# Kernel tuning notes

Hardware: AMD Instinct MI355X
Metric: run time of the kernel (lower is better)

## Reference

```python
import jax, jax.numpy as jnp
import numpy as np

B, S, DX, DH = 8, 4096, 1024, 1024

def setup_inputs() -> dict:
    key = jax.random.key(0)
    ks = jax.random.split(key, 7)
    s_x = 1.0 / np.sqrt(DX)
    s_h = 1.0 / np.sqrt(DH)
    return {
        "x":  jax.random.normal(ks[0], (B, S, DX), dtype=jnp.float32),
        "Wz": jax.random.uniform(ks[1], (DH, DX), jnp.float32, -s_x, s_x),
        "bz": jax.random.uniform(ks[2], (DH,),   jnp.float32, -s_x, s_x),
        "Wh": jax.random.uniform(ks[3], (DH, DX), jnp.float32, -s_x, s_x),
        "bh": jax.random.uniform(ks[4], (DH,),   jnp.float32, -s_x, s_x),
        "Wo": jax.random.uniform(ks[5], (DX, DH), jnp.float32, -s_h, s_h),
        "bo": jax.random.uniform(ks[6], (DX,),   jnp.float32, -s_h, s_h),
    }

def log_g(x):
    # Appendix B.3 of "Were RNNs All We Needed?"
    return jnp.where(x >= 0, jnp.log(jax.nn.relu(x) + 0.5), -jax.nn.softplus(-x))

def parallel_scan_log(log_coeffs, log_values):
    # Heinsen log-space associative scan: h_t = a_t * h_{t-1} + b_t (h_0 = 0)
    a_star = jnp.cumsum(log_coeffs, axis=1)                       # [B,S,H]
    log_h = a_star + jax.lax.cumlogsumexp(log_values - a_star, axis=1)
    return jnp.exp(log_h)

def reference(x, Wz, bz, Wh, bh, Wo, bo):
    k       = jnp.einsum('bsd,hd->bsh', x, Wz) + bz               # pre-gate
    tilde_h = jnp.einsum('bsd,hd->bsh', x, Wh) + bh               # candidate
    log_z           = -jax.nn.softplus(-k)                        # log sigmoid(k)
    log_one_minus_z = -jax.nn.softplus(k)                         # log sigmoid(-k)
    log_tilde_h     = log_g(tilde_h)
    h = parallel_scan_log(log_one_minus_z, log_z + log_tilde_h)   # [B,S,H]
    out = jnp.einsum('bsh,dh->bsd', h, Wo) + bo                   # [B,S,DX]
    return out
```

## Files before the change

### kernel.cpp

```cpp
#include <hip/hip_runtime.h>
#include <stdint.h>
#include <stddef.h>


typedef __bf16 bf16;
typedef __bf16 bf16x8 __attribute__((ext_vector_type(8)));
typedef float f32x4 __attribute__((ext_vector_type(4)));

#define DEV __device__ __forceinline__

DEV void gload_lds16(const bf16* g, bf16* l) {
  __builtin_amdgcn_global_load_lds((const __attribute__((address_space(1))) void*)g,
                                   (__attribute__((address_space(3))) void*)l,
                                   16, 0, 0);
}

__global__ __launch_bounds__(256)
void conv_b(const float* __restrict__ src, bf16* __restrict__ dst, int n4) {
  const int stride = gridDim.x * 256;
  for (int i = blockIdx.x * 256 + threadIdx.x; i < n4; i += stride) {
    float4 v = ((const float4*)src)[i];
    bf16 o[4] = {(bf16)v.x, (bf16)v.y, (bf16)v.z, (bf16)v.w};
    *(uint64_t*)(dst + 4 * (size_t)i) = *(uint64_t*)o;
  }
}

__global__ __launch_bounds__(256, 2)
void gate_gemm(const bf16* __restrict__ X,
               const bf16* __restrict__ Wz, const bf16* __restrict__ Wh,
               const float* __restrict__ bzf, const float* __restrict__ bhf,
               bf16* __restrict__ aB, bf16* __restrict__ vB) {
  __shared__ __align__(16) bf16 As [128 * 32];
  __shared__ __align__(16) bf16 Bzs[128 * 32];
  __shared__ __align__(16) bf16 Bhs[128 * 32];

  const int lane = threadIdx.x & 63;
  const int wave = threadIdx.x >> 6;
  const int wm = wave >> 1, wn = wave & 1;
  const int tileM = blockIdx.y * 128;
  const int tileN = blockIdx.x * 128;
  const int q = lane >> 4, r = lane & 15;
  const int srow = lane >> 2;
  const int scol = (lane & 3) * 8;

  const bf16* ga[2]; const bf16* gz[2]; const bf16* gh[2];
  bf16* la[2]; bf16* lz[2]; bf16* lh[2];
#pragma unroll
  for (int j = 0; j < 2; ++j) {
    const int cid = j * 4 + wave;
    const int row = cid * 16 + srow;
    ga[j] = X  + (size_t)(tileM + row) * 1024 + scol;
    gz[j] = Wz + (size_t)(tileN + row) * 1024 + scol;
    gh[j] = Wh + (size_t)(tileN + row) * 1024 + scol;
    la[j] = As  + cid * 512;
    lz[j] = Bzs + cid * 512;
    lh[j] = Bhs + cid * 512;
  }

  const bf16* pA[4]; const bf16* pBz[4]; const bf16* pBh[4];
#pragma unroll
  for (int f = 0; f < 4; ++f) {
    pA[f]  = As  + (wm * 64 + f * 16 + r) * 32 + q * 8;
    pBz[f] = Bzs + (wn * 64 + f * 16 + r) * 32 + q * 8;
    pBh[f] = Bhs + (wn * 64 + f * 16 + r) * 32 + q * 8;
  }

  f32x4 accz[4][4], acch[4][4];
#pragma unroll
  for (int i = 0; i < 4; ++i)
#pragma unroll
    for (int j = 0; j < 4; ++j) {
      accz[i][j] = (f32x4){0.f, 0.f, 0.f, 0.f};
      acch[i][j] = (f32x4){0.f, 0.f, 0.f, 0.f};
    }

  for (int k0 = 0; k0 < 1024; k0 += 32) {
    __syncthreads();
#pragma unroll
    for (int j = 0; j < 2; ++j) {
      gload_lds16(ga[j] + k0, la[j]);
      gload_lds16(gz[j] + k0, lz[j]);
      gload_lds16(gh[j] + k0, lh[j]);
    }
    __syncthreads();

    bf16x8 af[4];
#pragma unroll
    for (int fm = 0; fm < 4; ++fm) af[fm] = *(const bf16x8*)pA[fm];
#pragma unroll
    for (int fn = 0; fn < 4; ++fn) {
      bf16x8 bz8 = *(const bf16x8*)pBz[fn];
      bf16x8 bh8 = *(const bf16x8*)pBh[fn];
#pragma unroll
      for (int fm = 0; fm < 4; ++fm) {
        accz[fm][fn] = __builtin_amdgcn_mfma_f32_16x16x32_bf16(af[fm], bz8, accz[fm][fn], 0, 0, 0);
        acch[fm][fn] = __builtin_amdgcn_mfma_f32_16x16x32_bf16(af[fm], bh8, acch[fm][fn], 0, 0, 0);
      }
    }
  }

#pragma unroll
  for (int fn = 0; fn < 4; ++fn) {
    const int n = tileN + wn * 64 + fn * 16 + r;
    const float bzv = bzf[n], bhv = bhf[n];
#pragma unroll
    for (int fm = 0; fm < 4; ++fm) {
      const int m0 = tileM + wm * 64 + fm * 16 + q * 4;
#pragma unroll
      for (int i = 0; i < 4; ++i) {
        float kv = accz[fm][fn][i] + bzv;
        float tv = acch[fm][fn][i] + bhv;
        float e   = __expf(-kv);
        float inv = 1.f / (1.f + e);
        float a   = e * inv;
        float g   = (tv >= 0.f) ? (tv + 0.5f) : (1.f / (1.f + __expf(-tv)));
        size_t idx = (size_t)(m0 + i) * 1024 + n;
        aB[idx] = (bf16)a;
        vB[idx] = (bf16)(inv * g);
      }
    }
  }
}

__global__ __launch_bounds__(256)
void chk_gate(const bf16* __restrict__ X,
              const bf16* __restrict__ Wz, const bf16* __restrict__ Wh,
              const float* __restrict__ bzf, const float* __restrict__ bhf,
              const bf16* __restrict__ aB, const bf16* __restrict__ vB,
              int* __restrict__ badA) {
  int i = blockIdx.x * 256 + threadIdx.x;
  int m = (i * 12347) & 32767;
  int n = (i * 4099) & 1023;
  float kz = 0.f, kh = 0.f;
  for (int k = 0; k < 1024; ++k) {
    float xv = (float)X[(size_t)m * 1024 + k];
    kz = fmaf(xv, (float)Wz[(size_t)n * 1024 + k], kz);
    kh = fmaf(xv, (float)Wh[(size_t)n * 1024 + k], kh);
  }
  kz += bzf[n]; kh += bhf[n];
  float e = __expf(-kz), inv = 1.f / (1.f + e);
  float a = e * inv;
  float g = (kh >= 0.f) ? (kh + 0.5f) : (1.f / (1.f + __expf(-kh)));
  float v = inv * g;
  size_t idx = (size_t)m * 1024 + n;
  int ok = (fabsf((float)aB[idx] - a) <= 0.04f) &&
           (fabsf((float)vB[idx] - v) <= 0.08f);
  if (!ok) atomicAdd(badA, 1);
}

__global__ __launch_bounds__(256)
void fb_gate(const int* __restrict__ badA, const bf16* __restrict__ X,
             const bf16* __restrict__ Wz, const bf16* __restrict__ Wh,
             const float* __restrict__ bzf, const float* __restrict__ bhf,
             bf16* __restrict__ aB, bf16* __restrict__ vB) {
  if (*badA < 4) return;
  const int n = (blockIdx.x & 3) * 256 + threadIdx.x;
  const int m0 = (blockIdx.x >> 2) * 16;
  for (int mi = 0; mi < 16; ++mi) {
    const int m = m0 + mi;
    float kz = 0.f, kh = 0.f;
    for (int k = 0; k < 1024; ++k) {
      float xv = (float)X[(size_t)m * 1024 + k];
      kz = fmaf(xv, (float)Wz[(size_t)n * 1024 + k], kz);
      kh = fmaf(xv, (float)Wh[(size_t)n * 1024 + k], kh);
    }
    kz += bzf[n]; kh += bhf[n];
    float e = __expf(-kz), inv = 1.f / (1.f + e);
    float a = e * inv;
    float g = (kh >= 0.f) ? (kh + 0.5f) : (1.f / (1.f + __expf(-kh)));
    size_t idx = (size_t)m * 1024 + n;
    aB[idx] = (bf16)a;
    vB[idx] = (bf16)(inv * g);
  }
}

__global__ __launch_bounds__(256)
void scan_phase1(const bf16* __restrict__ aB, const bf16* __restrict__ vB,
                 float* __restrict__ Ac, float* __restrict__ Vc) {
  const int tid = blockIdx.x * 256 + threadIdx.x;
  const int hg = tid & 127, c = (tid >> 7) & 63, b = tid >> 13;
  const size_t base = (size_t)(b * 4096 + c * 64) * 1024 + hg * 8;
  float A[8], V[8];
#pragma unroll
  for (int j = 0; j < 8; ++j) { A[j] = 1.f; V[j] = 0.f; }
#pragma unroll 8
  for (int t = 0; t < 64; ++t) {
    bf16x8 a8 = *(const bf16x8*)(aB + base + (size_t)t * 1024);
    bf16x8 v8 = *(const bf16x8*)(vB + base + (size_t)t * 1024);
#pragma unroll
    for (int j = 0; j < 8; ++j) {
      float a = (float)a8[j];
      V[j] = fmaf(a, V[j], (float)v8[j]);
      A[j] *= a;
    }
  }
  const size_t o = (size_t)(b * 64 + c) * 1024 + hg * 8;
#pragma unroll
  for (int j = 0; j < 8; ++j) { Ac[o + j] = A[j]; Vc[o + j] = V[j]; }
}

__global__ __launch_bounds__(256)
void scan_phase2(const float* __restrict__ Ac, const float* __restrict__ Vc,
                 float* __restrict__ Hin) {
  const int tid = blockIdx.x * 256 + threadIdx.x;
  const int h = tid & 1023, b = tid >> 10;
  float carry = 0.f;
  for (int c = 0; c < 64; ++c) {
    const int idx = (b * 64 + c) * 1024 + h;
    Hin[idx] = carry;
    carry = fmaf(Ac[idx], carry, Vc[idx]);
  }
}

__global__ __launch_bounds__(256)
void scan_phase3(const bf16* __restrict__ aB, const bf16* vB,
                 const float* __restrict__ Hin, bf16* hB) {
  const int tid = blockIdx.x * 256 + threadIdx.x;
  const int hg = tid & 127, c = (tid >> 7) & 63, b = tid >> 13;
  const size_t base = (size_t)(b * 4096 + c * 64) * 1024 + hg * 8;
  const size_t o = (size_t)(b * 64 + c) * 1024 + hg * 8;
  float hc[8];
#pragma unroll
  for (int j = 0; j < 8; ++j) hc[j] = Hin[o + j];
#pragma unroll 4
  for (int t = 0; t < 64; ++t) {
    bf16x8 a8 = *(const bf16x8*)(aB + base + (size_t)t * 1024);
    bf16x8 v8 = *(const bf16x8*)(vB + base + (size_t)t * 1024);
    bf16x8 h8;
#pragma unroll
    for (int j = 0; j < 8; ++j) {
      hc[j] = fmaf((float)a8[j], hc[j], (float)v8[j]);
      h8[j] = (bf16)hc[j];
    }
    *(bf16x8*)(hB + base + (size_t)t * 1024) = h8;
  }
}

__global__ __launch_bounds__(256, 2)
void out_gemm(const bf16* __restrict__ H, const bf16* __restrict__ Wo,
              const float* __restrict__ bof, float* __restrict__ O) {
  __shared__ __align__(16) bf16 As[128 * 32];
  __shared__ __align__(16) bf16 Bs[128 * 32];

  const int lane = threadIdx.x & 63;
  const int wave = threadIdx.x >> 6;
  const int wm = wave >> 1, wn = wave & 1;
  const int tileM = blockIdx.y * 128;
  const int tileN = blockIdx.x * 128;
  const int q = lane >> 4, r = lane & 15;
  const int srow = lane >> 2;
  const int scol = (lane & 3) * 8;

  const bf16* ga[2]; const bf16* gb[2]; bf16* la[2]; bf16* lb[2];
#pragma unroll
  for (int j = 0; j < 2; ++j) {
    const int cid = j * 4 + wave;
    const int row = cid * 16 + srow;
    ga[j] = H  + (size_t)(tileM + row) * 1024 + scol;
    gb[j] = Wo + (size_t)(tileN + row) * 1024 + scol;
    la[j] = As + cid * 512;
    lb[j] = Bs + cid * 512;
  }
  const bf16* pA[4]; const bf16* pB[4];
#pragma unroll
  for (int f = 0; f < 4; ++f) {
    pA[f] = As + (wm * 64 + f * 16 + r) * 32 + q * 8;
    pB[f] = Bs + (wn * 64 + f * 16 + r) * 32 + q * 8;
  }

  f32x4 acc[4][4];
#pragma unroll
  for (int i = 0; i < 4; ++i)
#pragma unroll
    for (int j = 0; j < 4; ++j) acc[i][j] = (f32x4){0.f, 0.f, 0.f, 0.f};

  for (int k0 = 0; k0 < 1024; k0 += 32) {
    __syncthreads();
#pragma unroll
    for (int j = 0; j < 2; ++j) {
      gload_lds16(ga[j] + k0, la[j]);
      gload_lds16(gb[j] + k0, lb[j]);
    }
    __syncthreads();

    bf16x8 af[4];
#pragma unroll
    for (int fm = 0; fm < 4; ++fm) af[fm] = *(const bf16x8*)pA[fm];
#pragma unroll
    for (int fn = 0; fn < 4; ++fn) {
      bf16x8 b8 = *(const bf16x8*)pB[fn];
#pragma unroll
      for (int fm = 0; fm < 4; ++fm)
        acc[fm][fn] = __builtin_amdgcn_mfma_f32_16x16x32_bf16(af[fm], b8, acc[fm][fn], 0, 0, 0);
    }
  }

#pragma unroll
  for (int fn = 0; fn < 4; ++fn) {
    const int n = tileN + wn * 64 + fn * 16 + r;
    const float bov = bof[n];
#pragma unroll
    for (int fm = 0; fm < 4; ++fm) {
      const int m0 = tileM + wm * 64 + fm * 16 + q * 4;
#pragma unroll
      for (int i = 0; i < 4; ++i)
        O[(size_t)(m0 + i) * 1024 + n] = acc[fm][fn][i] + bov;
    }
  }
}

__global__ __launch_bounds__(256)
void chk_out(const bf16* __restrict__ H, const bf16* __restrict__ Wo,
             const float* __restrict__ bof, const float* __restrict__ O,
             int* __restrict__ badB) {
  int i = blockIdx.x * 256 + threadIdx.x;
  int m = (i * 12347) & 32767;
  int n = (i * 4099) & 1023;
  float acc = 0.f;
  for (int k = 0; k < 1024; ++k)
    acc = fmaf((float)H[(size_t)m * 1024 + k], (float)Wo[(size_t)n * 1024 + k], acc);
  acc += bof[n];
  int ok = fabsf(O[(size_t)m * 1024 + n] - acc) <= 0.05f;
  if (!ok) atomicAdd(badB, 1);
}

__global__ __launch_bounds__(256)
void fb_out(const int* __restrict__ badB, const bf16* __restrict__ H,
            const bf16* __restrict__ Wo, const float* __restrict__ bof,
            float* __restrict__ O) {
  if (*badB < 4) return;
  const int n = (blockIdx.x & 3) * 256 + threadIdx.x;
  const int m0 = (blockIdx.x >> 2) * 16;
  for (int mi = 0; mi < 16; ++mi) {
    const int m = m0 + mi;
    float acc = 0.f;
    for (int k = 0; k < 1024; ++k)
      acc = fmaf((float)H[(size_t)m * 1024 + k], (float)Wo[(size_t)n * 1024 + k], acc);
    O[(size_t)m * 1024 + n] = acc + bof[n];
  }
}

extern "C" void kernel_launch(void* const* d_in, const int* in_sizes, int n_in,
                              void* d_out, int out_size, void* d_ws, size_t ws_size,
                              hipStream_t stream) {
  char* ws = (char*)d_ws;
  bf16*  aB  = (bf16*)(ws);
  bf16*  vB  = (bf16*)(ws + 67108864ull);
  float* Ac  = (float*)(ws + 134217728ull);
  float* Vc  = (float*)(ws + 136314880ull);
  float* Hin = (float*)(ws + 138412032ull);
  int*   flags = (int*)(ws + 140509184ull);
  bf16*  wzb = (bf16*)(ws + 140525568ull);
  bf16*  whb = wzb + 1048576;
  bf16*  wob = whb + 1048576;
  bf16*  xb  = (bf16*)(ws + 148914176ull);

  const float* bzf = (const float*)d_in[2];
  const float* bhf = (const float*)d_in[4];
  const float* bof = (const float*)d_in[6];

  hipMemsetAsync(flags, 0, 8, stream);
  conv_b<<<32768, 256, 0, stream>>>((const float*)d_in[0], xb, 8388608);
  conv_b<<<1024,  256, 0, stream>>>((const float*)d_in[1], wzb, 262144);
  conv_b<<<1024,  256, 0, stream>>>((const float*)d_in[3], whb, 262144);
  conv_b<<<1024,  256, 0, stream>>>((const float*)d_in[5], wob, 262144);

  dim3 blk(256);
  dim3 gg(8, 256);

  gate_gemm<<<gg, blk, 0, stream>>>(xb, wzb, whb, bzf, bhf, aB, vB);
  chk_gate<<<4, blk, 0, stream>>>(xb, wzb, whb, bzf, bhf, aB, vB, flags);
  fb_gate<<<8192, blk, 0, stream>>>(flags, xb, wzb, whb, bzf, bhf, aB, vB);

  scan_phase1<<<256, blk, 0, stream>>>(aB, vB, Ac, Vc);
  scan_phase2<<<32,  blk, 0, stream>>>(Ac, Vc, Hin);
  scan_phase3<<<256, blk, 0, stream>>>(aB, vB, Hin, vB );

  out_gemm<<<gg, blk, 0, stream>>>(vB, wob, bof, (float*)d_out);
  chk_out<<<4, blk, 0, stream>>>(vB, wob, bof, (const float*)d_out, flags + 1);
  fb_out<<<8192, blk, 0, stream>>>(flags + 1, vB, wob, bof, (float*)d_out);
}
```

Before: 703.2 us.

## Double-buffer GEMM LDS loads, swizzle tiles per XCD, parallelize checks, fuse weight conversion

Both GEMMs now use two LDS buffers, so the next K-slice's global-to-LDS load is issued before computing the current slice. That leaves one barrier per iteration instead of two. Tile indices are remapped so that blocks landing on the same XCD share the same M rows, which should improve L2 reuse. The check kernels now use one wavefront per sample with a shuffle reduction instead of one serial thread per sample, the three weight conversions are merged into one launch, and the x conversion grid is smaller. The cost is doubled LDS use, which may reduce occupancy.

```diff
diff --git a/kernel.cpp b/kernel.cpp
--- a/kernel.cpp
+++ b/kernel.cpp
@@ -25,20 +25,44 @@
   }
 }
 
+__global__ __launch_bounds__(256)
+void conv_w3(const float* __restrict__ s0, const float* __restrict__ s1,
+             const float* __restrict__ s2,
+             bf16* __restrict__ d0, bf16* __restrict__ d1, bf16* __restrict__ d2) {
+  const int stride = gridDim.x * 256;
+  for (int i = blockIdx.x * 256 + threadIdx.x; i < 786432; i += stride) {
+    const float* s; bf16* d; int off;
+    if (i < 262144)      { s = s0; d = d0; off = i; }
+    else if (i < 524288) { s = s1; d = d1; off = i - 262144; }
+    else                 { s = s2; d = d2; off = i - 524288; }
+    float4 v = ((const float4*)s)[off];
+    bf16 o[4] = {(bf16)v.x, (bf16)v.y, (bf16)v.z, (bf16)v.w};
+    *(uint64_t*)(d + 4 * (size_t)off) = *(uint64_t*)o;
+  }
+}
+
+DEV void xcd_tiles(int bx, int by, int& tileM, int& tileN) {
+  const int d = by * 8 + bx;
+  const int xcd = d & 7;
+  const int i = d >> 3;
+  tileM = (xcd * 32 + (i >> 3)) * 128;
+  tileN = (i & 7) * 128;
+}
+
 __global__ __launch_bounds__(256, 2)
 void gate_gemm(const bf16* __restrict__ X,
                const bf16* __restrict__ Wz, const bf16* __restrict__ Wh,
                const float* __restrict__ bzf, const float* __restrict__ bhf,
                bf16* __restrict__ aB, bf16* __restrict__ vB) {
-  __shared__ __align__(16) bf16 As [128 * 32];
-  __shared__ __align__(16) bf16 Bzs[128 * 32];
-  __shared__ __align__(16) bf16 Bhs[128 * 32];
+  __shared__ __align__(16) bf16 As [2 * 4096];
+  __shared__ __align__(16) bf16 Bzs[2 * 4096];
+  __shared__ __align__(16) bf16 Bhs[2 * 4096];
 
   const int lane = threadIdx.x & 63;
   const int wave = threadIdx.x >> 6;
   const int wm = wave >> 1, wn = wave & 1;
-  const int tileM = blockIdx.y * 128;
-  const int tileN = blockIdx.x * 128;
+  int tileM, tileN;
+  xcd_tiles(blockIdx.x, blockIdx.y, tileM, tileN);
   const int q = lane >> 4, r = lane & 15;
   const int srow = lane >> 2;
   const int scol = (lane & 3) * 8;
@@ -74,30 +98,42 @@
       acch[i][j] = (f32x4){0.f, 0.f, 0.f, 0.f};
     }
 
-  for (int k0 = 0; k0 < 1024; k0 += 32) {
-    __syncthreads();
+  auto STAGE = [&](int buf, int k0) {
+    const int bo = buf * 4096;
 #pragma unroll
     for (int j = 0; j < 2; ++j) {
-      gload_lds16(ga[j] + k0, la[j]);
-      gload_lds16(gz[j] + k0, lz[j]);
-      gload_lds16(gh[j] + k0, lh[j]);
-    }
-    __syncthreads();
-
+      gload_lds16(ga[j] + k0, la[j] + bo);
+      gload_lds16(gz[j] + k0, lz[j] + bo);
+      gload_lds16(gh[j] + k0, lh[j] + bo);
+    }
+  };
+  auto COMPUTE = [&](int buf) {
+    const int bo = buf * 4096;
     bf16x8 af[4];
 #pragma unroll
-    for (int fm = 0; fm < 4; ++fm) af[fm] = *(const bf16x8*)pA[fm];
+    for (int fm = 0; fm < 4; ++fm) af[fm] = *(const bf16x8*)(pA[fm] + bo);
 #pragma unroll
     for (int fn = 0; fn < 4; ++fn) {
-      bf16x8 bz8 = *(const bf16x8*)pBz[fn];
-      bf16x8 bh8 = *(const bf16x8*)pBh[fn];
+      bf16x8 bz8 = *(const bf16x8*)(pBz[fn] + bo);
+      bf16x8 bh8 = *(const bf16x8*)(pBh[fn] + bo);
 #pragma unroll
       for (int fm = 0; fm < 4; ++fm) {
         accz[fm][fn] = __builtin_amdgcn_mfma_f32_16x16x32_bf16(af[fm], bz8, accz[fm][fn], 0, 0, 0);
         acch[fm][fn] = __builtin_amdgcn_mfma_f32_16x16x32_bf16(af[fm], bh8, acch[fm][fn], 0, 0, 0);
       }
     }
-  }
+  };
+
+  STAGE(0, 0);
+  int cur = 0;
+  for (int t = 0; t < 31; ++t) {
+    __syncthreads();
+    STAGE(cur ^ 1, (t + 1) * 32);
+    COMPUTE(cur);
+    cur ^= 1;
+  }
+  __syncthreads();
+  COMPUTE(cur);
 
 #pragma unroll
   for (int fn = 0; fn < 4; ++fn) {
@@ -128,24 +164,32 @@
               const float* __restrict__ bzf, const float* __restrict__ bhf,
               const bf16* __restrict__ aB, const bf16* __restrict__ vB,
               int* __restrict__ badA) {
-  int i = blockIdx.x * 256 + threadIdx.x;
-  int m = (i * 12347) & 32767;
-  int n = (i * 4099) & 1023;
+  const int w = (blockIdx.x * 256 + threadIdx.x) >> 6;
+  const int lane = threadIdx.x & 63;
+  const int m = (w * 12347) & 32767;
+  const int n = (w * 4099) & 1023;
   float kz = 0.f, kh = 0.f;
-  for (int k = 0; k < 1024; ++k) {
+  for (int k = lane; k < 1024; k += 64) {
     float xv = (float)X[(size_t)m * 1024 + k];
     kz = fmaf(xv, (float)Wz[(size_t)n * 1024 + k], kz);
     kh = fmaf(xv, (float)Wh[(size_t)n * 1024 + k], kh);
   }
-  kz += bzf[n]; kh += bhf[n];
-  float e = __expf(-kz), inv = 1.f / (1.f + e);
-  float a = e * inv;
-  float g = (kh >= 0.f) ? (kh + 0.5f) : (1.f / (1.f + __expf(-kh)));
-  float v = inv * g;
-  size_t idx = (size_t)m * 1024 + n;
-  int ok = (fabsf((float)aB[idx] - a) <= 0.04f) &&
-           (fabsf((float)vB[idx] - v) <= 0.08f);
-  if (!ok) atomicAdd(badA, 1);
+#pragma unroll
+  for (int off = 32; off; off >>= 1) {
+    kz += __shfl_xor(kz, off);
+    kh += __shfl_xor(kh, off);
+  }
+  if (lane == 0) {
+    kz += bzf[n]; kh += bhf[n];
+    float e = __expf(-kz), inv = 1.f / (1.f + e);
+    float a = e * inv;
+    float g = (kh >= 0.f) ? (kh + 0.5f) : (1.f / (1.f + __expf(-kh)));
+    float v = inv * g;
+    size_t idx = (size_t)m * 1024 + n;
+    int ok = (fabsf((float)aB[idx] - a) <= 0.04f) &&
+             (fabsf((float)vB[idx] - v) <= 0.08f);
+    if (!ok) atomicAdd(badA, 1);
+  }
 }
 
 __global__ __launch_bounds__(256)
@@ -239,14 +283,14 @@
 __global__ __launch_bounds__(256, 2)
 void out_gemm(const bf16* __restrict__ H, const bf16* __restrict__ Wo,
               const float* __restrict__ bof, float* __restrict__ O) {
-  __shared__ __align__(16) bf16 As[128 * 32];
-  __shared__ __align__(16) bf16 Bs[128 * 32];
+  __shared__ __align__(16) bf16 As[2 * 4096];
+  __shared__ __align__(16) bf16 Bs[2 * 4096];
 
   const int lane = threadIdx.x & 63;
   const int wave = threadIdx.x >> 6;
   const int wm = wave >> 1, wn = wave & 1;
-  const int tileM = blockIdx.y * 128;
-  const int tileN = blockIdx.x * 128;
+  int tileM, tileN;
+  xcd_tiles(blockIdx.x, blockIdx.y, tileM, tileN);
   const int q = lane >> 4, r = lane & 15;
   const int srow = lane >> 2;
   const int scol = (lane & 3) * 8;
@@ -274,26 +318,38 @@
 #pragma unroll
     for (int j = 0; j < 4; ++j) acc[i][j] = (f32x4){0.f, 0.f, 0.f, 0.f};
 
-  for (int k0 = 0; k0 < 1024; k0 += 32) {
-    __syncthreads();
+  auto STAGE = [&](int buf, int k0) {
+    const int bo = buf * 4096;
 #pragma unroll
     for (int j = 0; j < 2; ++j) {
-      gload_lds16(ga[j] + k0, la[j]);
-      gload_lds16(gb[j] + k0, lb[j]);
-    }
-    __syncthreads();
-
+      gload_lds16(ga[j] + k0, la[j] + bo);
+      gload_lds16(gb[j] + k0, lb[j] + bo);
+    }
+  };
+  auto COMPUTE = [&](int buf) {
+    const int bo = buf * 4096;
     bf16x8 af[4];
 #pragma unroll
-    for (int fm = 0; fm < 4; ++fm) af[fm] = *(const bf16x8*)pA[fm];
+    for (int fm = 0; fm < 4; ++fm) af[fm] = *(const bf16x8*)(pA[fm] + bo);
 #pragma unroll
     for (int fn = 0; fn < 4; ++fn) {
-      bf16x8 b8 = *(const bf16x8*)pB[fn];
+      bf16x8 b8 = *(const bf16x8*)(pB[fn] + bo);
 #pragma unroll
       for (int fm = 0; fm < 4; ++fm)
         acc[fm][fn] = __builtin_amdgcn_mfma_f32_16x16x32_bf16(af[fm], b8, acc[fm][fn], 0, 0, 0);
     }
-  }
+  };
+
+  STAGE(0, 0);
+  int cur = 0;
+  for (int t = 0; t < 31; ++t) {
+    __syncthreads();
+    STAGE(cur ^ 1, (t + 1) * 32);
+    COMPUTE(cur);
+    cur ^= 1;
+  }
+  __syncthreads();
+  COMPUTE(cur);
 
 #pragma unroll
   for (int fn = 0; fn < 4; ++fn) {
@@ -313,15 +369,20 @@
 void chk_out(const bf16* __restrict__ H, const bf16* __restrict__ Wo,
              const float* __restrict__ bof, const float* __restrict__ O,
              int* __restrict__ badB) {
-  int i = blockIdx.x * 256 + threadIdx.x;
-  int m = (i * 12347) & 32767;
-  int n = (i * 4099) & 1023;
+  const int w = (blockIdx.x * 256 + threadIdx.x) >> 6;
+  const int lane = threadIdx.x & 63;
+  const int m = (w * 12347) & 32767;
+  const int n = (w * 4099) & 1023;
   float acc = 0.f;
-  for (int k = 0; k < 1024; ++k)
+  for (int k = lane; k < 1024; k += 64)
     acc = fmaf((float)H[(size_t)m * 1024 + k], (float)Wo[(size_t)n * 1024 + k], acc);
-  acc += bof[n];
-  int ok = fabsf(O[(size_t)m * 1024 + n] - acc) <= 0.05f;
-  if (!ok) atomicAdd(badB, 1);
+#pragma unroll
+  for (int off = 32; off; off >>= 1) acc += __shfl_xor(acc, off);
+  if (lane == 0) {
+    acc += bof[n];
+    int ok = fabsf(O[(size_t)m * 1024 + n] - acc) <= 0.05f;
+    if (!ok) atomicAdd(badB, 1);
+  }
 }
 
 __global__ __launch_bounds__(256)
@@ -360,16 +421,15 @@
   const float* bof = (const float*)d_in[6];
 
   hipMemsetAsync(flags, 0, 8, stream);
-  conv_b<<<32768, 256, 0, stream>>>((const float*)d_in[0], xb, 8388608);
-  conv_b<<<1024,  256, 0, stream>>>((const float*)d_in[1], wzb, 262144);
-  conv_b<<<1024,  256, 0, stream>>>((const float*)d_in[3], whb, 262144);
-  conv_b<<<1024,  256, 0, stream>>>((const float*)d_in[5], wob, 262144);
+  conv_b<<<4096, 256, 0, stream>>>((const float*)d_in[0], xb, 8388608);
+  conv_w3<<<3072, 256, 0, stream>>>((const float*)d_in[1], (const float*)d_in[3],
+                                    (const float*)d_in[5], wzb, whb, wob);
 
   dim3 blk(256);
   dim3 gg(8, 256);
 
   gate_gemm<<<gg, blk, 0, stream>>>(xb, wzb, whb, bzf, bhf, aB, vB);
-  chk_gate<<<4, blk, 0, stream>>>(xb, wzb, whb, bzf, bhf, aB, vB, flags);
+  chk_gate<<<256, blk, 0, stream>>>(xb, wzb, whb, bzf, bhf, aB, vB, flags);
   fb_gate<<<8192, blk, 0, stream>>>(flags, xb, wzb, whb, bzf, bhf, aB, vB);
 
   scan_phase1<<<256, blk, 0, stream>>>(aB, vB, Ac, Vc);
@@ -377,6 +437,6 @@
   scan_phase3<<<256, blk, 0, stream>>>(aB, vB, Hin, vB );
 
   out_gemm<<<gg, blk, 0, stream>>>(vB, wob, bof, (float*)d_out);
-  chk_out<<<4, blk, 0, stream>>>(vB, wob, bof, (const float*)d_out, flags + 1);
+  chk_out<<<256, blk, 0, stream>>>(vB, wob, bof, (const float*)d_out, flags + 1);
   fb_out<<<8192, blk, 0, stream>>>(flags + 1, vB, wob, bof, (float*)d_out);
 }
```

New measurement: 620.6 us. 11.7% less time.
